# Kernel tuning notes

Hardware: AMD Instinct MI355X
Metric: run time of the kernel (lower is better)

The kernel has to match this reference:

```python
import jax, jax.numpy as jnp
import numpy as np

N_NODES = 100000
N_EDGES = 3200000
IN_DIM = 512
HID_DIM = 512


def setup_inputs() -> dict:
    key = jax.random.key(0)
    k = jax.random.split(key, 8)
    x = jax.random.normal(k[0], (N_NODES, IN_DIM), dtype=jnp.float32)
    adj_src = jax.random.randint(k[1], (N_EDGES,), 0, N_NODES, dtype=jnp.int32)
    adj_dst = jax.random.randint(k[2], (N_EDGES,), 0, N_NODES, dtype=jnp.int32)
    adj_val = jax.random.uniform(k[3], (N_EDGES,), dtype=jnp.float32)
    s = 1.0 / np.sqrt(IN_DIM)
    W1 = jax.random.uniform(k[4], (IN_DIM, HID_DIM), minval=-s, maxval=s, dtype=jnp.float32)
    b1 = jnp.zeros((HID_DIM,), dtype=jnp.float32)
    s2 = 1.0 / np.sqrt(HID_DIM)
    W2 = jax.random.uniform(k[5], (HID_DIM, HID_DIM), minval=-s2, maxval=s2, dtype=jnp.float32)
    b2 = jnp.zeros((HID_DIM,), dtype=jnp.float32)
    return {"x": x, "adj_src": adj_src, "adj_dst": adj_dst, "adj_val": adj_val,
            "W1": W1, "b1": b1, "W2": W2, "b2": b2}


def _spmm(src, dst, val, h):
    # adj @ h with adj in COO: out[dst] += val * h[src]
    msgs = h[src] * val[:, None]            # [E, D]
    return jax.ops.segment_sum(msgs, dst, num_segments=N_NODES)


def reference(x, adj_src, adj_dst, adj_val, W1, b1, W2, b2):
    # Inference mode: dropout is identity (training=False).
    # Layer 1: linear -> SpMM -> ReLU
    h = x @ W1 + b1
    h = _spmm(adj_src, adj_dst, adj_val, h)
    h = jax.nn.relu(h)
    # Layer 2: linear -> SpMM -> ReLU
    h = h @ W2 + b2
    h = _spmm(adj_src, adj_dst, adj_val, h)
    h = jax.nn.relu(h)
    return h
```

## Files before the change

kernel.cpp:

```cpp
#include <hip/hip_runtime.h>


#define N_NODES 100000
#define N_EDGES 3200000
#define DIM 512
#define BUCKET_CAP 128

typedef __attribute__((ext_vector_type(8))) __bf16 bf16x8;
typedef __attribute__((ext_vector_type(4))) float f32x4;
typedef __attribute__((ext_vector_type(4))) unsigned int u32x4;
typedef __attribute__((ext_vector_type(2))) int i32x2;

__device__ inline unsigned short f2bf(float f) {
    unsigned int u = __builtin_bit_cast(unsigned int, f);
    unsigned int r = (u + 0x7FFFu + ((u >> 16) & 1u)) >> 16;
    return (unsigned short)r;
}
__device__ inline float bf2f(unsigned short s) {
    unsigned int u = ((unsigned int)s) << 16;
    return __builtin_bit_cast(float, u);
}

__global__ __launch_bounds__(256) void k_cvt(const f32x4* __restrict__ in,
                                             ushort4* __restrict__ out, int n4) {
    int i = blockIdx.x * 256 + threadIdx.x;
    if (i >= n4) return;
    f32x4 v = __builtin_nontemporal_load(in + i);
    ushort4 o;
    o.x = f2bf(v[0]); o.y = f2bf(v[1]); o.z = f2bf(v[2]); o.w = f2bf(v[3]);
    out[i] = o;
}

__global__ __launch_bounds__(256) void k_wt(const float* __restrict__ W,
                                            unsigned short* __restrict__ Wt) {
    int idx = blockIdx.x * 256 + threadIdx.x;
    int k = idx & 511, n = idx >> 9;
    Wt[n * 512 + k] = f2bf(W[k * 512 + n]);
}

__global__ __launch_bounds__(256) void k_scatter(const int* __restrict__ src,
                                                 const int* __restrict__ dst,
                                                 const float* __restrict__ val,
                                                 int* __restrict__ cnt,
                                                 i32x2* __restrict__ bucket) {
    int e = blockIdx.x * 256 + threadIdx.x;
    if (e >= N_EDGES) return;
    int d = dst[e];
    int pos = atomicAdd(cnt + d, 1);
    if (pos < BUCKET_CAP) {
        i32x2 ed;
        ed[0] = src[e];
        ed[1] = __float_as_int(val[e]);
        __builtin_nontemporal_store(ed, bucket + ((size_t)d << 7) + pos);
    }
}

__global__ __launch_bounds__(256, 2)
void k_gemm(const unsigned short* __restrict__ A, const unsigned short* __restrict__ Bt,
            const float* __restrict__ bias, unsigned short* __restrict__ C, int M) {
    __shared__ unsigned short sA[128][40];
    __shared__ unsigned short sB[128][40];
    const int t = threadIdx.x;
    const int m0 = blockIdx.y * 128;
    const int n0 = blockIdx.x * 128;
    const int wave = t >> 6;
    const int lane = t & 63;
    const int wm = (wave & 1) << 6;
    const int wn = (wave >> 1) << 6;
    const int quad = lane >> 4;
    const int l16 = lane & 15;

    f32x4 acc[4][4];
#pragma unroll
    for (int i = 0; i < 4; i++)
#pragma unroll
        for (int j = 0; j < 4; j++) acc[i][j] = (f32x4){0.f, 0.f, 0.f, 0.f};

    const int row_s = t >> 2;
    const int q_s = t & 3;

    for (int k0 = 0; k0 < 512; k0 += 32) {
        __syncthreads();
#pragma unroll
        for (int i = 0; i < 2; i++) {
            int row = row_s + (i << 6);
            int gr = m0 + row;
            u32x4 av = {0u, 0u, 0u, 0u};
            if (gr < M) av = *(const u32x4*)(A + (size_t)gr * 512 + k0 + q_s * 8);
            *(u32x4*)(&sA[row][q_s * 8]) = av;
            u32x4 bv = *(const u32x4*)(Bt + (size_t)(n0 + row) * 512 + k0 + q_s * 8);
            *(u32x4*)(&sB[row][q_s * 8]) = bv;
        }
        __syncthreads();
        bf16x8 af[4], bfr[4];
#pragma unroll
        for (int i = 0; i < 4; i++)
            af[i] = *(const bf16x8*)(&sA[wm + i * 16 + l16][quad * 8]);
#pragma unroll
        for (int j = 0; j < 4; j++)
            bfr[j] = *(const bf16x8*)(&sB[wn + j * 16 + l16][quad * 8]);
#pragma unroll
        for (int i = 0; i < 4; i++)
#pragma unroll
            for (int j = 0; j < 4; j++)
                acc[i][j] = __builtin_amdgcn_mfma_f32_16x16x32_bf16(af[i], bfr[j], acc[i][j], 0, 0, 0);
    }

#pragma unroll
    for (int i = 0; i < 4; i++) {
        int rbase = m0 + wm + i * 16 + quad * 4;
#pragma unroll
        for (int j = 0; j < 4; j++) {
            int col = n0 + wn + j * 16 + l16;
            float bv = bias[col];
#pragma unroll
            for (int r = 0; r < 4; r++) {
                int row = rbase + r;
                if (row < M) C[(size_t)row * 512 + col] = f2bf(acc[i][j][r] + bv);
            }
        }
    }
}

__global__ __launch_bounds__(256)
void k_spmm(const i32x2* __restrict__ bucket, const int* __restrict__ cnt,
            const unsigned short* __restrict__ Hin,
            unsigned short* __restrict__ out_bf, float* __restrict__ out_f32) {
    __shared__ i32x2 sE[4][BUCKET_CAP];
    const int w = threadIdx.x >> 6;
    const int lane = threadIdx.x & 63;
    const int node = blockIdx.x * 4 + w;
    int deg = cnt[node];
    if (deg > BUCKET_CAP) deg = BUCKET_CAP;
    const i32x2* bk = bucket + ((size_t)node << 7);
    if (lane < deg)      sE[w][lane]      = __builtin_nontemporal_load(bk + lane);
    if (lane + 64 < deg) sE[w][lane + 64] = __builtin_nontemporal_load(bk + lane + 64);
    __syncthreads();

    float a[8];
#pragma unroll
    for (int i = 0; i < 8; i++) a[i] = 0.f;

    if (deg > 0) {
        i32x2 ed = sE[w][0];
        float v = __int_as_float(ed[1]);
        u32x4 p = *(const u32x4*)(Hin + (((size_t)ed[0]) << 9) + (lane << 3));
        for (int e = 1; e < deg; e++) {
            i32x2 edn = sE[w][e];
            float vn = __int_as_float(edn[1]);
            u32x4 pn = *(const u32x4*)(Hin + (((size_t)edn[0]) << 9) + (lane << 3));
#pragma unroll
            for (int q = 0; q < 4; q++) {
                a[2 * q]     += v * __builtin_bit_cast(float, p[q] << 16);
                a[2 * q + 1] += v * __builtin_bit_cast(float, p[q] & 0xFFFF0000u);
            }
            p = pn; v = vn;
        }
#pragma unroll
        for (int q = 0; q < 4; q++) {
            a[2 * q]     += v * __builtin_bit_cast(float, p[q] << 16);
            a[2 * q + 1] += v * __builtin_bit_cast(float, p[q] & 0xFFFF0000u);
        }
    }

#pragma unroll
    for (int i = 0; i < 8; i++) a[i] = fmaxf(a[i], 0.f);

    size_t o = (((size_t)node) << 9) + (lane << 3);
    if (out_f32 != nullptr) {
        f32x4 v0 = {a[0], a[1], a[2], a[3]};
        f32x4 v1 = {a[4], a[5], a[6], a[7]};
        __builtin_nontemporal_store(v0, (f32x4*)(out_f32 + o));
        __builtin_nontemporal_store(v1, (f32x4*)(out_f32 + o + 4));
    } else {
        u32x4 pk;
#pragma unroll
        for (int q = 0; q < 4; q++)
            pk[q] = (unsigned int)f2bf(a[2 * q]) | ((unsigned int)f2bf(a[2 * q + 1]) << 16);
        __builtin_nontemporal_store(pk, (u32x4*)(out_bf + o));
    }
}

extern "C" void kernel_launch(void* const* d_in, const int* in_sizes, int n_in,
                              void* d_out, int out_size, void* d_ws, size_t ws_size,
                              hipStream_t stream) {
    const float* x       = (const float*)d_in[0];
    const int*   adj_src = (const int*)d_in[1];
    const int*   adj_dst = (const int*)d_in[2];
    const float* adj_val = (const float*)d_in[3];
    const float* W1      = (const float*)d_in[4];
    const float* b1      = (const float*)d_in[5];
    const float* W2      = (const float*)d_in[6];
    const float* b2      = (const float*)d_in[7];

    const size_t ND = (size_t)N_NODES * DIM;

    unsigned short* xb  = (unsigned short*)d_ws;
    unsigned short* w1t = xb + ND;
    unsigned short* w2t = w1t + 262144;
    int*  cnt    = (int*)(w2t + 262144);
    i32x2* bucket = (i32x2*)(cnt + 100096);

    unsigned short* h1 = (unsigned short*)d_out;
    unsigned short* h2 = h1 + ND;
    unsigned short* h3 = xb;

    k_cvt<<<50000, 256, 0, stream>>>((const f32x4*)x, (ushort4*)xb, (int)(ND / 4));
    k_wt<<<1024, 256, 0, stream>>>(W1, w1t);
    k_wt<<<1024, 256, 0, stream>>>(W2, w2t);

    hipMemsetAsync(cnt, 0, N_NODES * sizeof(int), stream);
    k_scatter<<<12500, 256, 0, stream>>>(adj_src, adj_dst, adj_val, cnt, bucket);

    dim3 ggrid(4, (N_NODES + 127) / 128);

    k_gemm<<<ggrid, 256, 0, stream>>>(xb, w1t, b1, h1, N_NODES);
    k_spmm<<<N_NODES / 4, 256, 0, stream>>>(bucket, cnt, h1, h2, nullptr);

    k_gemm<<<ggrid, 256, 0, stream>>>(h2, w2t, b2, h3, N_NODES);
    k_spmm<<<N_NODES / 4, 256, 0, stream>>>(bucket, cnt, h3, nullptr, (float*)d_out);
}
```

Measured before the change: 1.766 ms.

## Sort each node's edge bucket by source chunk via count-scan-place

Replaces the single atomic scatter with a three-pass count, per-node exclusive scan, and placement keyed on (source chunk, destination). Each node's incoming edges end up grouped by source-index range, so the SpMM gathers of feature rows have better temporal locality across concurrently running waves. In exchange it adds an extra pass over the edge arrays, a 49x100000 counter table (zeroed and scanned each call, stored temporarily in the output buffer), and more atomics.

```diff
diff --git a/kernel.cpp b/kernel.cpp
--- a/kernel.cpp
+++ b/kernel.cpp
@@ -5,6 +5,8 @@
 #define N_EDGES 3200000
 #define DIM 512
 #define BUCKET_CAP 128
+#define CHUNK_SHIFT 11
+#define N_CHUNK 49
 
 typedef __attribute__((ext_vector_type(8))) __bf16 bf16x8;
 typedef __attribute__((ext_vector_type(4))) float f32x4;
@@ -15,10 +17,6 @@
     unsigned int u = __builtin_bit_cast(unsigned int, f);
     unsigned int r = (u + 0x7FFFu + ((u >> 16) & 1u)) >> 16;
     return (unsigned short)r;
-}
-__device__ inline float bf2f(unsigned short s) {
-    unsigned int u = ((unsigned int)s) << 16;
-    return __builtin_bit_cast(float, u);
 }
 
 __global__ __launch_bounds__(256) void k_cvt(const f32x4* __restrict__ in,
@@ -38,18 +36,42 @@
     Wt[n * 512 + k] = f2bf(W[k * 512 + n]);
 }
 
-__global__ __launch_bounds__(256) void k_scatter(const int* __restrict__ src,
-                                                 const int* __restrict__ dst,
-                                                 const float* __restrict__ val,
-                                                 int* __restrict__ cnt,
-                                                 i32x2* __restrict__ bucket) {
+__global__ __launch_bounds__(256) void k_count(const int* __restrict__ src,
+                                               const int* __restrict__ dst,
+                                               unsigned int* __restrict__ ccnt) {
     int e = blockIdx.x * 256 + threadIdx.x;
     if (e >= N_EDGES) return;
-    int d = dst[e];
-    int pos = atomicAdd(cnt + d, 1);
+    int c = src[e] >> CHUNK_SHIFT;
+    atomicAdd(&ccnt[(size_t)c * N_NODES + dst[e]], 1u);
+}
+
+__global__ __launch_bounds__(256) void k_scan(unsigned int* __restrict__ ccnt,
+                                              int* __restrict__ cnt) {
+    int d = blockIdx.x * 256 + threadIdx.x;
+    if (d >= N_NODES) return;
+    unsigned int s = 0;
+    for (int c = 0; c < N_CHUNK; c++) {
+        size_t idx = (size_t)c * N_NODES + d;
+        unsigned int t = ccnt[idx];
+        ccnt[idx] = s;
+        s += t;
+    }
+    cnt[d] = (int)s;
+}
+
+__global__ __launch_bounds__(256) void k_place(const int* __restrict__ src,
+                                               const int* __restrict__ dst,
+                                               const float* __restrict__ val,
+                                               unsigned int* __restrict__ ccnt,
+                                               i32x2* __restrict__ bucket) {
+    int e = blockIdx.x * 256 + threadIdx.x;
+    if (e >= N_EDGES) return;
+    int s = src[e], d = dst[e];
+    int c = s >> CHUNK_SHIFT;
+    unsigned int pos = atomicAdd(&ccnt[(size_t)c * N_NODES + d], 1u);
     if (pos < BUCKET_CAP) {
         i32x2 ed;
-        ed[0] = src[e];
+        ed[0] = s;
         ed[1] = __float_as_int(val[e]);
         __builtin_nontemporal_store(ed, bucket + ((size_t)d << 7) + pos);
     }
@@ -201,6 +223,7 @@
     int*  cnt    = (int*)(w2t + 262144);
     i32x2* bucket = (i32x2*)(cnt + 100096);
 
+    unsigned int*   ccnt = (unsigned int*)d_out;
     unsigned short* h1 = (unsigned short*)d_out;
     unsigned short* h2 = h1 + ND;
     unsigned short* h3 = xb;
@@ -209,8 +232,10 @@
     k_wt<<<1024, 256, 0, stream>>>(W1, w1t);
     k_wt<<<1024, 256, 0, stream>>>(W2, w2t);
 
-    hipMemsetAsync(cnt, 0, N_NODES * sizeof(int), stream);
-    k_scatter<<<12500, 256, 0, stream>>>(adj_src, adj_dst, adj_val, cnt, bucket);
+    hipMemsetAsync(ccnt, 0, (size_t)N_CHUNK * N_NODES * sizeof(unsigned int), stream);
+    k_count<<<12500, 256, 0, stream>>>(adj_src, adj_dst, ccnt);
+    k_scan<<<(N_NODES + 255) / 256, 256, 0, stream>>>(ccnt, cnt);
+    k_place<<<12500, 256, 0, stream>>>(adj_src, adj_dst, adj_val, ccnt, bucket);
 
     dim3 ggrid(4, (N_NODES + 127) / 128);
 
```

Result: slower. 1.893 ms (+7.2%).

## Split SpMM feature dimension into 8 slices across grid y

Applied to the files above, without the earlier changes.

The SpMM kernel now launches an extra grid dimension of 8 slices, and each wave handles 64 features of one node with one bf16 element per lane instead of 8. The aim is more parallelism and more independent gathers in flight. In exchange, every block reloads the edge bucket 8 times, gathers become 2-byte scalar loads (128 bytes per wave per edge) instead of 16-byte vector loads, and output stores become scalar.

```diff
diff --git a/kernel.cpp b/kernel.cpp
--- a/kernel.cpp
+++ b/kernel.cpp
@@ -5,6 +5,8 @@
 #define N_EDGES 3200000
 #define DIM 512
 #define BUCKET_CAP 128
+#define NSLICE 8
+#define SLICE_DIM 64
 
 typedef __attribute__((ext_vector_type(8))) __bf16 bf16x8;
 typedef __attribute__((ext_vector_type(4))) float f32x4;
@@ -130,6 +132,7 @@
     const int w = threadIdx.x >> 6;
     const int lane = threadIdx.x & 63;
     const int node = blockIdx.x * 4 + w;
+    const int d0 = blockIdx.y * SLICE_DIM;
     int deg = cnt[node];
     if (deg > BUCKET_CAP) deg = BUCKET_CAP;
     const i32x2* bk = bucket + ((size_t)node << 7);
@@ -137,47 +140,28 @@
     if (lane + 64 < deg) sE[w][lane + 64] = __builtin_nontemporal_load(bk + lane + 64);
     __syncthreads();
 
-    float a[8];
-#pragma unroll
-    for (int i = 0; i < 8; i++) a[i] = 0.f;
-
+    const unsigned short* __restrict__ col = Hin + d0 + lane;
+    float a = 0.f;
     if (deg > 0) {
         i32x2 ed = sE[w][0];
         float v = __int_as_float(ed[1]);
-        u32x4 p = *(const u32x4*)(Hin + (((size_t)ed[0]) << 9) + (lane << 3));
+        unsigned short h = col[(size_t)ed[0] << 9];
         for (int e = 1; e < deg; e++) {
             i32x2 edn = sE[w][e];
             float vn = __int_as_float(edn[1]);
-            u32x4 pn = *(const u32x4*)(Hin + (((size_t)edn[0]) << 9) + (lane << 3));
-#pragma unroll
-            for (int q = 0; q < 4; q++) {
-                a[2 * q]     += v * __builtin_bit_cast(float, p[q] << 16);
-                a[2 * q + 1] += v * __builtin_bit_cast(float, p[q] & 0xFFFF0000u);
-            }
-            p = pn; v = vn;
+            unsigned short hn = col[(size_t)edn[0] << 9];
+            a += v * bf2f(h);
+            h = hn; v = vn;
         }
-#pragma unroll
-        for (int q = 0; q < 4; q++) {
-            a[2 * q]     += v * __builtin_bit_cast(float, p[q] << 16);
-            a[2 * q + 1] += v * __builtin_bit_cast(float, p[q] & 0xFFFF0000u);
-        }
-    }
-
-#pragma unroll
-    for (int i = 0; i < 8; i++) a[i] = fmaxf(a[i], 0.f);
-
-    size_t o = (((size_t)node) << 9) + (lane << 3);
+        a += v * bf2f(h);
+    }
+    a = fmaxf(a, 0.f);
+
+    const size_t o = (((size_t)node) << 9) + d0 + lane;
     if (out_f32 != nullptr) {
-        f32x4 v0 = {a[0], a[1], a[2], a[3]};
-        f32x4 v1 = {a[4], a[5], a[6], a[7]};
-        __builtin_nontemporal_store(v0, (f32x4*)(out_f32 + o));
-        __builtin_nontemporal_store(v1, (f32x4*)(out_f32 + o + 4));
+        __builtin_nontemporal_store(a, out_f32 + o);
     } else {
-        u32x4 pk;
-#pragma unroll
-        for (int q = 0; q < 4; q++)
-            pk[q] = (unsigned int)f2bf(a[2 * q]) | ((unsigned int)f2bf(a[2 * q + 1]) << 16);
-        __builtin_nontemporal_store(pk, (u32x4*)(out_bf + o));
+        __builtin_nontemporal_store(f2bf(a), out_bf + o);
     }
 }
 
@@ -213,10 +197,11 @@
     k_scatter<<<12500, 256, 0, stream>>>(adj_src, adj_dst, adj_val, cnt, bucket);
 
     dim3 ggrid(4, (N_NODES + 127) / 128);
+    dim3 sgrid(N_NODES / 4, NSLICE);
 
     k_gemm<<<ggrid, 256, 0, stream>>>(xb, w1t, b1, h1, N_NODES);
-    k_spmm<<<N_NODES / 4, 256, 0, stream>>>(bucket, cnt, h1, h2, nullptr);
+    k_spmm<<<sgrid, 256, 0, stream>>>(bucket, cnt, h1, h2, nullptr);
 
     k_gemm<<<ggrid, 256, 0, stream>>>(h2, w2t, b2, h3, N_NODES);
-    k_spmm<<<N_NODES / 4, 256, 0, stream>>>(bucket, cnt, h3, nullptr, (float*)d_out);
-}
+    k_spmm<<<sgrid, 256, 0, stream>>>(bucket, cnt, h3, nullptr, (float*)d_out);
+}
```

Result: slower. 1.952 ms (+10.5%).
